# Kernel tuning notes

Measured on AMD Instinct MI355X. Metric: run time of the kernel, lower is better.

## Reference

```python
import jax, jax.numpy as jnp
import numpy as np

N_ASSETS = 128
N_FEATURES = 128
BATCH = 32
N_ITERS = 500      # fixed-iteration OSQP-style ADMM (replaces CVXPY/OSQP solve)
RHO = 0.1          # ADMM penalty
SIGMA = 1e-6       # primal regularization (OSQP default scale)
RELAX = 1.6        # over-relaxation
ALPHA = 0.5        # self.alpha (EN mix)
DELTA = 10.0       # risk aversion (forward default)
NEG_INF = -1e20


def setup_inputs() -> dict:
    key = jax.random.key(0)
    ks = jax.random.split(key, 3)
    X = jax.random.normal(ks[0], (BATCH, N_FEATURES), jnp.float32)
    F = jax.random.normal(ks[1], (N_ASSETS, N_ASSETS), jnp.float32)
    V = (F @ F.T) / N_ASSETS + 0.1 * jnp.eye(N_ASSETS, dtype=jnp.float32)  # PSD covariance
    beta = 0.1 * jax.random.normal(ks[2], (N_FEATURES, N_ASSETS), jnp.float32)
    theta_E = jnp.zeros((N_ASSETS,), jnp.float32)
    theta_D = jnp.zeros((N_ASSETS,), jnp.float32)
    log_gamma1 = jnp.zeros((), jnp.float32)
    log_gamma2 = jnp.zeros((), jnp.float32)
    A = jnp.ones((1, N_ASSETS), jnp.float32)        # budget: sum(z) == 1
    b = jnp.ones((1,), jnp.float32)
    G = -jnp.eye(N_ASSETS, dtype=jnp.float32)       # long-only: -z <= 0
    h = jnp.zeros((N_ASSETS,), jnp.float32)
    return dict(X=X, V=V, beta=beta, theta_E=theta_E, theta_D=theta_D,
                log_gamma1=log_gamma1, log_gamma2=log_gamma2, A=A, b=b, G=G, h=h)


def _forward(X, V, beta, theta_E, theta_D, log_gamma1, log_gamma2, A, b, G, h):
    n = V.shape[0]
    y_pred = X @ beta                                  # (B, n)
    gamma1 = 10.0 ** log_gamma1
    gamma2 = 10.0 ** log_gamma2
    d = jax.nn.sigmoid(theta_D)                        # diag(D)
    e = jax.nn.sigmoid(theta_E)                        # diag(E)
    Q_reg = DELTA * V + (1.0 - ALPHA) * gamma2 * jnp.diag(d * d)
    # L1 split z = u_plus - u_minus, u >= 0 -> augmented QP in u of size 2n
    Q_aug = jnp.block([[Q_reg, -Q_reg], [-Q_reg, Q_reg]])   # (2n, 2n)
    p_term = ALPHA * gamma1 * e                        # alpha*gamma1*colsum(E^T) with E diagonal
    # p_i = -y_pred[i]; p_aug = [p + p_term, -p + p_term]
    P = jnp.concatenate([-y_pred + p_term[None, :], y_pred + p_term[None, :]], axis=1)  # (B, 2n)
    # constraints: [A,-A] u == b ; [G,-G] u <= h ; -I u <= 0
    C = jnp.concatenate([
        jnp.concatenate([A, -A], axis=1),
        jnp.concatenate([G, -G], axis=1),
        -jnp.eye(2 * n, dtype=V.dtype),
    ], axis=0)                                         # (m, 2n), m = m_eq + n + 2n
    m_eq = A.shape[0]
    lo = jnp.concatenate([b, jnp.full((C.shape[0] - m_eq,), NEG_INF, V.dtype)])
    up = jnp.concatenate([b, h, jnp.zeros((2 * n,), V.dtype)])
    # OSQP ADMM with KKT reduced to an SPD system, factorized ONCE and shared across batch
    nz = 2 * n
    M = Q_aug + SIGMA * jnp.eye(nz, dtype=V.dtype) + RHO * (C.T @ C)
    L = jnp.linalg.cholesky(M)
    mC = C.shape[0]

    def solve_one(p):
        def step(carry, _):
            x, z, y = carry
            rhs = SIGMA * x - p + C.T @ (RHO * z - y)
            x_t = jax.scipy.linalg.cho_solve((L, True), rhs)
            z_t = C @ x_t
            x_new = RELAX * x_t + (1.0 - RELAX) * x
            z_r = RELAX * z_t + (1.0 - RELAX) * z
            z_new = jnp.clip(z_r + y / RHO, lo, up)
            y_new = y + RHO * (z_r - z_new)
            return (x_new, z_new, y_new), None
        init = (jnp.zeros((nz,), p.dtype), jnp.zeros((mC,), p.dtype), jnp.zeros((mC,), p.dtype))
        (x, _, _), _ = jax.lax.scan(step, init, None, length=N_ITERS)
        return x

    u = jax.vmap(solve_one)(P)                         # (B, 2n)
    z_batch = u[:, :n] - u[:, n:]                      # recover signed weights
    return z_batch, y_pred


def reference(X, V, beta, theta_E, theta_D, log_gamma1, log_gamma2, A, b, G, h):
    return _forward(X, V, beta, theta_E, theta_D, log_gamma1, log_gamma2, A, b, G, h)
```

## Files before the change

kernel.cpp:

```cpp
#include <hip/hip_runtime.h>

#define N 128
#define BATCH 32
#define N_SEG1 88
#define N_SEGM 16
#define N_CG 24

static constexpr float RHO_     = 0.1f;
static constexpr float SIGMA_   = 1e-6f;
static constexpr float RELAX_   = 1.9f;
static constexpr float ALPHA_   = 0.5f;
static constexpr float DELTA_   = 10.0f;
static constexpr float LN10_    = 2.302585092994046f;


__device__ __forceinline__ float rdlane(float v, int l) {
    return __builtin_bit_cast(float,
        __builtin_amdgcn_readlane(__builtin_bit_cast(int, v), l));
}
template <int CTRL, int RMASK>
__device__ __forceinline__ float dppadd(float v) {
    int r = __builtin_amdgcn_update_dpp(0, __builtin_bit_cast(int, v),
                                        CTRL, RMASK, 0xf, true);
    return v + __builtin_bit_cast(float, r);
}
__device__ __forceinline__ float wave_sum64(float v) {
    v = dppadd<0x111, 0xf>(v);
    v = dppadd<0x112, 0xf>(v);
    v = dppadd<0x114, 0xf>(v);
    v = dppadd<0x118, 0xf>(v);
    v = dppadd<0x142, 0xa>(v);
    v = dppadd<0x143, 0xc>(v);
    return rdlane(v, 63);
}

__global__ __launch_bounds__(256, 1) void k_front(
    const float* __restrict__ V, const float* __restrict__ thD,
    const float* __restrict__ lg2p, const float* __restrict__ Ag,
    float* __restrict__ H, float* __restrict__ wv)
{
    __shared__ alignas(16) float qs[2][2][N];

    const int tid  = threadIdx.x;
    const int c    = blockIdx.x;
    const int lane = tid & 63;
    const int wav4 = tid >> 6;
    const int i    = tid & 127;
    const int s    = tid >> 7;
    const int jb   = s * 64;

    float breg[64];
    {
        float ai   = Ag[i];
        float g2   = expf(lg2p[0] * LN10_);
        float di   = 1.0f / (1.0f + expf(-thD[i]));
        float diag = 2.0f * RHO_
                   + 2.0f * (1.0f - ALPHA_) * g2 * di * di
                   + (SIGMA_ + RHO_);
        float t2r  = 2.0f * RHO_ * ai;
        const float4* vp = (const float4*)(V + i * N + jb);
        const float4* ap = (const float4*)(Ag + jb);
#pragma unroll
        for (int j4 = 0; j4 < 16; ++j4) {
            float4 v4 = vp[j4], a4 = ap[j4];
            breg[4 * j4 + 0] = fmaf(2.0f * DELTA_, v4.x, t2r * a4.x)
                             + ((jb + 4 * j4 + 0 == i) ? diag : 0.f);
            breg[4 * j4 + 1] = fmaf(2.0f * DELTA_, v4.y, t2r * a4.y)
                             + ((jb + 4 * j4 + 1 == i) ? diag : 0.f);
            breg[4 * j4 + 2] = fmaf(2.0f * DELTA_, v4.z, t2r * a4.z)
                             + ((jb + 4 * j4 + 2 == i) ? diag : 0.f);
            breg[4 * j4 + 3] = fmaf(2.0f * DELTA_, v4.w, t2r * a4.w)
                             + ((jb + 4 * j4 + 3 == i) ? diag : 0.f);
        }
    }

    float x0 = 0.f, x1 = 0.f;
    float r0 = (c < N) ? ((lane == c) ? 1.f : 0.f) : Ag[lane];
    float r1 = (c < N) ? ((lane + 64 == c) ? 1.f : 0.f) : Ag[lane + 64];
    float p0 = r0, p1 = r1;
    float rr = wave_sum64(fmaf(r0, r0, r1 * r1));

    for (int it = 0; it < N_CG; ++it) {
        const int par = it & 1;
        {
            float psel = s ? p1 : p0;
            float a0 = 0.f, a1 = 0.f, a2 = 0.f, a3 = 0.f;
#pragma unroll
            for (int j = 0; j < 64; j += 4) {
                a0 = fmaf(breg[j + 0], rdlane(psel, j + 0), a0);
                a1 = fmaf(breg[j + 1], rdlane(psel, j + 1), a1);
                a2 = fmaf(breg[j + 2], rdlane(psel, j + 2), a2);
                a3 = fmaf(breg[j + 3], rdlane(psel, j + 3), a3);
            }
            qs[par][s][i] = (a0 + a1) + (a2 + a3);
        }
        __syncthreads();
        float q0 = qs[par][0][lane]      + qs[par][1][lane];
        float q1 = qs[par][0][lane + 64] + qs[par][1][lane + 64];
        float spq = wave_sum64(fmaf(p0, q0, p1 * q1));
        float srq = wave_sum64(fmaf(r0, q0, r1 * q1));
        float sqq = wave_sum64(fmaf(q0, q0, q1 * q1));
        float alpha = rr / fmaxf(spq, 1e-30f);
        x0 = fmaf(alpha, p0, x0); x1 = fmaf(alpha, p1, x1);
        r0 = fmaf(-alpha, q0, r0); r1 = fmaf(-alpha, q1, r1);
        float rrn = fmaf(alpha * alpha, sqq, fmaf(-2.0f * alpha, srq, rr));
        rrn = fmaxf(rrn, 0.f);
        float beta_ = rrn / fmaxf(rr, 1e-30f);
        rr = rrn;
        p0 = fmaf(beta_, p0, r0); p1 = fmaf(beta_, p1, r1);
    }
    if (wav4 == 0) {
        if (c < N) { H[c * N + lane] = x0; H[c * N + lane + 64] = x1; }
        else       { wv[lane] = x0; wv[lane + 64] = x1; }
    }
}

__global__ __launch_bounds__(256, 1) void k_admm(
    const float* __restrict__ Hg, const float* __restrict__ wg,
    const float* __restrict__ Ag, const float* __restrict__ bvec,
    const float* __restrict__ hvec, const float* __restrict__ X,
    const float* __restrict__ betag, const float* __restrict__ thE,
    const float* __restrict__ lg1p, float* __restrict__ out)
{
    __shared__ float pps[2][2][N];
    __shared__ float wzs[2][2];
    __shared__ float Xs[N];
    __shared__ float reds[4][3];

    int tid = threadIdx.x, b = blockIdx.x;
    const int lane = tid & 63;
    const int wav4 = tid >> 6;
    const int i    = tid & 127;
    const int s    = tid >> 7;
    const int jb   = s * 64;
    const int r    = jb + lane;

    if (tid < N) Xs[tid] = X[b * N + tid];
    __syncthreads();
    float y = 0.f;
#pragma unroll 8
    for (int k = 0; k < N; ++k)
        y = fmaf(Xs[k], betag[k * N + r], y);
    float gamma1 = expf(lg1p[0] * LN10_);
    float e  = 1.0f / (1.0f + expf(-thE[r]));
    float pt = ALPHA_ * gamma1 * e;
    float p1_i = -y + pt;
    float p2_i =  y + pt;
    if ((wav4 & 1) == 0)
        out[BATCH * N + b * N + r] = y;

    float hreg[64];
    {
        const float4* hp = (const float4*)(Hg + i * N + jb);
#pragma unroll
        for (int j4 = 0; j4 < 16; ++j4) {
            float4 v4 = hp[j4];
            hreg[4 * j4 + 0] = v4.x; hreg[4 * j4 + 1] = v4.y;
            hreg[4 * j4 + 2] = v4.z; hreg[4 * j4 + 3] = v4.w;
        }
    }
    float wl = wg[r];
    float b0 = bvec[0];

    float a_i  = Ag[r];
    float h_i  = hvec[r];
    float x1 = 0.f, x2 = 0.f;
    float z0 = 0.f, y0 = 0.f;
    float zg = 0.f, yg = 0.f;
    float zi1 = 0.f, yi1 = 0.f;
    float zi2 = 0.f, yi2 = 0.f;
    float svr = -p1_i - p2_i;
    float dl  = -p1_i + p2_i;

    const float inv_sr  = 1.0f / (SIGMA_ + RHO_);
    const float inv_rho = 1.0f / RHO_;
    const float cR = 1.0f - RELAX_;
    const float R2 = 0.5f * RELAX_;

#define ADMM_ITER(PAR)                                                    \
    {                                                                     \
        const int par = (PAR);                                            \
        if ((wav4 & 1) == 0) {                                            \
            float zp = wave_sum64(wl * dl);                               \
            if (lane == 0) wzs[par][s] = zp;                              \
        }                                                                 \
        float a0 = 0.f, a1 = 0.f, a2 = 0.f, a3 = 0.f;                     \
        _Pragma("unroll")                                                 \
        for (int j = 0; j < 64; j += 4) {                                 \
            a0 = fmaf(hreg[j + 0], rdlane(dl, j + 0), a0);                \
            a1 = fmaf(hreg[j + 1], rdlane(dl, j + 1), a1);                \
            a2 = fmaf(hreg[j + 2], rdlane(dl, j + 2), a2);                \
            a3 = fmaf(hreg[j + 3], rdlane(dl, j + 3), a3);                \
        }                                                                 \
        pps[par][s][i] = (a0 + a1) + (a2 + a3);                           \
        __syncthreads();                                                  \
        float xd  = pps[par][0][r] + pps[par][1][r];                      \
        float zt0 = wzs[par][0] + wzs[par][1];                            \
        float xs  = svr * inv_sr;                                         \
        float sd1 = xs + xd;                                              \
        float sd2 = xs - xd;                                              \
        x1 = fmaf(R2, sd1, cR * x1);                                      \
        x2 = fmaf(R2, sd2, cR * x2);                                      \
        float zr0 = fmaf(RELAX_, zt0, cR * z0);                           \
        y0 = fmaf(RHO_, zr0 - b0, y0); z0 = b0;                           \
        float zrg = fmaf(-RELAX_, xd, cR * zg);                           \
        float zng = fminf(fmaf(yg, inv_rho, zrg), h_i);                   \
        yg = fmaf(RHO_, zrg - zng, yg); zg = zng;                         \
        float zr1 = fmaf(-R2, sd1, cR * zi1);                             \
        float zn1 = fminf(fmaf(yi1, inv_rho, zr1), 0.f);                  \
        yi1 = fmaf(RHO_, zr1 - zn1, yi1); zi1 = zn1;                      \
        float zr2 = fmaf(-R2, sd2, cR * zi2);                             \
        float zn2 = fminf(fmaf(yi2, inv_rho, zr2), 0.f);                  \
        yi2 = fmaf(RHO_, zr2 - zn2, yi2); zi2 = zn2;                      \
        float t0  = fmaf(RHO_, z0,  -y0);                                 \
        float tg  = fmaf(RHO_, zg,  -yg);                                 \
        float tI1 = fmaf(RHO_, zi1, -yi1);                                \
        float tI2 = fmaf(RHO_, zi2, -yi2);                                \
        float g  = fmaf(a_i, t0, -tg);                                    \
        float r1 = fmaf(SIGMA_, x1, -p1_i) + g - tI1;                     \
        float r2 = fmaf(SIGMA_, x2, -p2_i) - g - tI2;                     \
        svr = r1 + r2;                                                    \
        dl  = r1 - r2;                                                    \
    }

    for (int it = 0; it < N_SEG1; ++it) ADMM_ITER(it & 1)
    float zA = x1 - x2;
    for (int it = 0; it < N_SEGM; ++it) ADMM_ITER(it & 1)
    float zB = x1 - x2;
    for (int it = 0; it < N_SEGM; ++it) ADMM_ITER(it & 1)
    float zC = x1 - x2;
#undef ADMM_ITER

    float d1 = zB - zA;
    float d2 = zC - zB;
    float s21 = wave_sum64(d2 * d1);
    float s11 = wave_sum64(d1 * d1);
    float s22 = wave_sum64(d2 * d2);
    if (lane == 0) {
        reds[wav4][0] = s21; reds[wav4][1] = s11; reds[wav4][2] = s22;
    }
    __syncthreads();
    float d21 = reds[0][0] + reds[1][0] + reds[2][0] + reds[3][0];
    float d11 = reds[0][1] + reds[1][1] + reds[2][1] + reds[3][1];
    float d22 = reds[0][2] + reds[1][2] + reds[2][2] + reds[3][2];
    float lam16 = fminf(d21 / fmaxf(d11, 1e-30f), 0.98f);
    bool  ok = (d21 > 0.f) && (d21 * d21 > 0.81f * d11 * d22)
             && (lam16 > 0.f);
    float fac  = lam16 / (1.0f - lam16);
    float zout = ok ? fmaf(d2, fac, zC) : zC;
    if ((wav4 & 1) == 0)
        out[b * N + r] = zout;
}

extern "C" void kernel_launch(void* const* d_in, const int* in_sizes, int n_in,
                              void* d_out, int out_size, void* d_ws, size_t ws_size,
                              hipStream_t stream) {
    (void)in_sizes; (void)n_in; (void)out_size; (void)ws_size;
    const float* X    = (const float*)d_in[0];
    const float* V    = (const float*)d_in[1];
    const float* beta = (const float*)d_in[2];
    const float* thE  = (const float*)d_in[3];
    const float* thD  = (const float*)d_in[4];
    const float* lg1  = (const float*)d_in[5];
    const float* lg2  = (const float*)d_in[6];
    const float* A    = (const float*)d_in[7];
    const float* bv   = (const float*)d_in[8];
    const float* hv   = (const float*)d_in[10];
    float* out = (float*)d_out;
    float* ws  = (float*)d_ws;
    float* Hm = ws;
    float* wv = ws + 16384;

    hipLaunchKernelGGL(k_front, dim3(N + 1), dim3(256), 0, stream,
                       V, thD, lg2, A, Hm, wv);
    hipLaunchKernelGGL(k_admm,  dim3(BATCH), dim3(256), 0, stream,
                       Hm, wv, A, bv, hv, X, beta, thE, lg1, out);
}
```

Before: 149.3 us.

## Fuse front CG and ADMM kernels into one cooperative launch with grid sync

Merges the CG-based inverse construction kernel and the batched ADMM kernel into a single cooperative kernel. Blocks beyond the front range compute y_pred and the linear terms while the front blocks run CG, then a grid-wide sync makes H available. This removes one launch and the inter-kernel gap and overlaps the prediction matmul with the CG work. In exchange it pays the cost of a cooperative launch and a grid barrier, and the front blocks idle-exit afterwards.

```diff
diff --git a/kernel.cpp b/kernel.cpp
--- a/kernel.cpp
+++ b/kernel.cpp
@@ -1,7 +1,11 @@
 #include <hip/hip_runtime.h>
+#include <hip/hip_cooperative_groups.h>
+
+namespace cg = cooperative_groups;
 
 #define N 128
 #define BATCH 32
+#define NFRONT (N + 1)
 #define N_SEG1 88
 #define N_SEGM 16
 #define N_CG 24
@@ -34,100 +38,23 @@
     return rdlane(v, 63);
 }
 
-__global__ __launch_bounds__(256, 1) void k_front(
+__global__ __launch_bounds__(256, 1) void k_fused(
     const float* __restrict__ V, const float* __restrict__ thD,
     const float* __restrict__ lg2p, const float* __restrict__ Ag,
-    float* __restrict__ H, float* __restrict__ wv)
+    float* __restrict__ Hws, float* __restrict__ wvws,
+    const float* __restrict__ bvec, const float* __restrict__ hvec,
+    const float* __restrict__ X, const float* __restrict__ betag,
+    const float* __restrict__ thE, const float* __restrict__ lg1p,
+    float* __restrict__ out)
 {
     __shared__ alignas(16) float qs[2][2][N];
-
-    const int tid  = threadIdx.x;
-    const int c    = blockIdx.x;
-    const int lane = tid & 63;
-    const int wav4 = tid >> 6;
-    const int i    = tid & 127;
-    const int s    = tid >> 7;
-    const int jb   = s * 64;
-
-    float breg[64];
-    {
-        float ai   = Ag[i];
-        float g2   = expf(lg2p[0] * LN10_);
-        float di   = 1.0f / (1.0f + expf(-thD[i]));
-        float diag = 2.0f * RHO_
-                   + 2.0f * (1.0f - ALPHA_) * g2 * di * di
-                   + (SIGMA_ + RHO_);
-        float t2r  = 2.0f * RHO_ * ai;
-        const float4* vp = (const float4*)(V + i * N + jb);
-        const float4* ap = (const float4*)(Ag + jb);
-#pragma unroll
-        for (int j4 = 0; j4 < 16; ++j4) {
-            float4 v4 = vp[j4], a4 = ap[j4];
-            breg[4 * j4 + 0] = fmaf(2.0f * DELTA_, v4.x, t2r * a4.x)
-                             + ((jb + 4 * j4 + 0 == i) ? diag : 0.f);
-            breg[4 * j4 + 1] = fmaf(2.0f * DELTA_, v4.y, t2r * a4.y)
-                             + ((jb + 4 * j4 + 1 == i) ? diag : 0.f);
-            breg[4 * j4 + 2] = fmaf(2.0f * DELTA_, v4.z, t2r * a4.z)
-                             + ((jb + 4 * j4 + 2 == i) ? diag : 0.f);
-            breg[4 * j4 + 3] = fmaf(2.0f * DELTA_, v4.w, t2r * a4.w)
-                             + ((jb + 4 * j4 + 3 == i) ? diag : 0.f);
-        }
-    }
-
-    float x0 = 0.f, x1 = 0.f;
-    float r0 = (c < N) ? ((lane == c) ? 1.f : 0.f) : Ag[lane];
-    float r1 = (c < N) ? ((lane + 64 == c) ? 1.f : 0.f) : Ag[lane + 64];
-    float p0 = r0, p1 = r1;
-    float rr = wave_sum64(fmaf(r0, r0, r1 * r1));
-
-    for (int it = 0; it < N_CG; ++it) {
-        const int par = it & 1;
-        {
-            float psel = s ? p1 : p0;
-            float a0 = 0.f, a1 = 0.f, a2 = 0.f, a3 = 0.f;
-#pragma unroll
-            for (int j = 0; j < 64; j += 4) {
-                a0 = fmaf(breg[j + 0], rdlane(psel, j + 0), a0);
-                a1 = fmaf(breg[j + 1], rdlane(psel, j + 1), a1);
-                a2 = fmaf(breg[j + 2], rdlane(psel, j + 2), a2);
-                a3 = fmaf(breg[j + 3], rdlane(psel, j + 3), a3);
-            }
-            qs[par][s][i] = (a0 + a1) + (a2 + a3);
-        }
-        __syncthreads();
-        float q0 = qs[par][0][lane]      + qs[par][1][lane];
-        float q1 = qs[par][0][lane + 64] + qs[par][1][lane + 64];
-        float spq = wave_sum64(fmaf(p0, q0, p1 * q1));
-        float srq = wave_sum64(fmaf(r0, q0, r1 * q1));
-        float sqq = wave_sum64(fmaf(q0, q0, q1 * q1));
-        float alpha = rr / fmaxf(spq, 1e-30f);
-        x0 = fmaf(alpha, p0, x0); x1 = fmaf(alpha, p1, x1);
-        r0 = fmaf(-alpha, q0, r0); r1 = fmaf(-alpha, q1, r1);
-        float rrn = fmaf(alpha * alpha, sqq, fmaf(-2.0f * alpha, srq, rr));
-        rrn = fmaxf(rrn, 0.f);
-        float beta_ = rrn / fmaxf(rr, 1e-30f);
-        rr = rrn;
-        p0 = fmaf(beta_, p0, r0); p1 = fmaf(beta_, p1, r1);
-    }
-    if (wav4 == 0) {
-        if (c < N) { H[c * N + lane] = x0; H[c * N + lane + 64] = x1; }
-        else       { wv[lane] = x0; wv[lane + 64] = x1; }
-    }
-}
-
-__global__ __launch_bounds__(256, 1) void k_admm(
-    const float* __restrict__ Hg, const float* __restrict__ wg,
-    const float* __restrict__ Ag, const float* __restrict__ bvec,
-    const float* __restrict__ hvec, const float* __restrict__ X,
-    const float* __restrict__ betag, const float* __restrict__ thE,
-    const float* __restrict__ lg1p, float* __restrict__ out)
-{
     __shared__ float pps[2][2][N];
     __shared__ float wzs[2][2];
     __shared__ float Xs[N];
     __shared__ float reds[4][3];
 
-    int tid = threadIdx.x, b = blockIdx.x;
+    const int cb   = blockIdx.x;
+    const int tid  = threadIdx.x;
     const int lane = tid & 63;
     const int wav4 = tid >> 6;
     const int i    = tid & 127;
@@ -135,23 +62,100 @@
     const int jb   = s * 64;
     const int r    = jb + lane;
 
-    if (tid < N) Xs[tid] = X[b * N + tid];
-    __syncthreads();
-    float y = 0.f;
+    float p1_i = 0.f, p2_i = 0.f;
+
+    if (cb < NFRONT) {
+        const int c = cb;
+        float breg[64];
+        {
+            float ai   = Ag[i];
+            float g2   = expf(lg2p[0] * LN10_);
+            float di   = 1.0f / (1.0f + expf(-thD[i]));
+            float diag = 2.0f * RHO_
+                       + 2.0f * (1.0f - ALPHA_) * g2 * di * di
+                       + (SIGMA_ + RHO_);
+            float t2r  = 2.0f * RHO_ * ai;
+            const float4* vp = (const float4*)(V + i * N + jb);
+            const float4* ap = (const float4*)(Ag + jb);
+#pragma unroll
+            for (int j4 = 0; j4 < 16; ++j4) {
+                float4 v4 = vp[j4], a4 = ap[j4];
+                breg[4 * j4 + 0] = fmaf(2.0f * DELTA_, v4.x, t2r * a4.x)
+                                 + ((jb + 4 * j4 + 0 == i) ? diag : 0.f);
+                breg[4 * j4 + 1] = fmaf(2.0f * DELTA_, v4.y, t2r * a4.y)
+                                 + ((jb + 4 * j4 + 1 == i) ? diag : 0.f);
+                breg[4 * j4 + 2] = fmaf(2.0f * DELTA_, v4.z, t2r * a4.z)
+                                 + ((jb + 4 * j4 + 2 == i) ? diag : 0.f);
+                breg[4 * j4 + 3] = fmaf(2.0f * DELTA_, v4.w, t2r * a4.w)
+                                 + ((jb + 4 * j4 + 3 == i) ? diag : 0.f);
+            }
+        }
+        float x0 = 0.f, x1 = 0.f;
+        float r0 = (c < N) ? ((lane == c) ? 1.f : 0.f) : Ag[lane];
+        float r1 = (c < N) ? ((lane + 64 == c) ? 1.f : 0.f) : Ag[lane + 64];
+        float p0 = r0, p1 = r1;
+        float rr = wave_sum64(fmaf(r0, r0, r1 * r1));
+
+        for (int it = 0; it < N_CG; ++it) {
+            const int par = it & 1;
+            {
+                float psel = s ? p1 : p0;
+                float a0 = 0.f, a1 = 0.f, a2 = 0.f, a3 = 0.f;
+#pragma unroll
+                for (int j = 0; j < 64; j += 4) {
+                    a0 = fmaf(breg[j + 0], rdlane(psel, j + 0), a0);
+                    a1 = fmaf(breg[j + 1], rdlane(psel, j + 1), a1);
+                    a2 = fmaf(breg[j + 2], rdlane(psel, j + 2), a2);
+                    a3 = fmaf(breg[j + 3], rdlane(psel, j + 3), a3);
+                }
+                qs[par][s][i] = (a0 + a1) + (a2 + a3);
+            }
+            __syncthreads();
+            float q0 = qs[par][0][lane]      + qs[par][1][lane];
+            float q1 = qs[par][0][lane + 64] + qs[par][1][lane + 64];
+            float spq = wave_sum64(fmaf(p0, q0, p1 * q1));
+            float srq = wave_sum64(fmaf(r0, q0, r1 * q1));
+            float sqq = wave_sum64(fmaf(q0, q0, q1 * q1));
+            float alpha = rr / fmaxf(spq, 1e-30f);
+            x0 = fmaf(alpha, p0, x0); x1 = fmaf(alpha, p1, x1);
+            r0 = fmaf(-alpha, q0, r0); r1 = fmaf(-alpha, q1, r1);
+            float rrn = fmaf(alpha * alpha, sqq,
+                             fmaf(-2.0f * alpha, srq, rr));
+            rrn = fmaxf(rrn, 0.f);
+            float beta_ = rrn / fmaxf(rr, 1e-30f);
+            rr = rrn;
+            p0 = fmaf(beta_, p0, r0); p1 = fmaf(beta_, p1, r1);
+        }
+        if (wav4 == 0) {
+            if (c < N) { Hws[c * N + lane] = x0; Hws[c * N + lane + 64] = x1; }
+            else       { wvws[lane] = x0; wvws[lane + 64] = x1; }
+        }
+    } else {
+        const int b = cb - NFRONT;
+        if (tid < N) Xs[tid] = X[b * N + tid];
+        __syncthreads();
+        float y = 0.f;
 #pragma unroll 8
-    for (int k = 0; k < N; ++k)
-        y = fmaf(Xs[k], betag[k * N + r], y);
-    float gamma1 = expf(lg1p[0] * LN10_);
-    float e  = 1.0f / (1.0f + expf(-thE[r]));
-    float pt = ALPHA_ * gamma1 * e;
-    float p1_i = -y + pt;
-    float p2_i =  y + pt;
-    if ((wav4 & 1) == 0)
-        out[BATCH * N + b * N + r] = y;
-
+        for (int k = 0; k < N; ++k)
+            y = fmaf(Xs[k], betag[k * N + r], y);
+        float gamma1 = expf(lg1p[0] * LN10_);
+        float e  = 1.0f / (1.0f + expf(-thE[r]));
+        float pt = ALPHA_ * gamma1 * e;
+        p1_i = -y + pt;
+        p2_i =  y + pt;
+        if ((wav4 & 1) == 0)
+            out[BATCH * N + b * N + r] = y;
+    }
+
+    __threadfence();
+    cg::this_grid().sync();
+    if (cb < NFRONT) return;
+    __threadfence();
+
+    const int b = cb - NFRONT;
     float hreg[64];
     {
-        const float4* hp = (const float4*)(Hg + i * N + jb);
+        const float4* hp = (const float4*)(Hws + i * N + jb);
 #pragma unroll
         for (int j4 = 0; j4 < 16; ++j4) {
             float4 v4 = hp[j4];
@@ -159,9 +163,8 @@
             hreg[4 * j4 + 2] = v4.z; hreg[4 * j4 + 3] = v4.w;
         }
     }
-    float wl = wg[r];
+    float wl = wvws[r];
     float b0 = bvec[0];
-
     float a_i  = Ag[r];
     float h_i  = hvec[r];
     float x1 = 0.f, x2 = 0.f;
@@ -271,8 +274,10 @@
     float* Hm = ws;
     float* wv = ws + 16384;
 
-    hipLaunchKernelGGL(k_front, dim3(N + 1), dim3(256), 0, stream,
-                       V, thD, lg2, A, Hm, wv);
-    hipLaunchKernelGGL(k_admm,  dim3(BATCH), dim3(256), 0, stream,
-                       Hm, wv, A, bv, hv, X, beta, thE, lg1, out);
-}
+    void* args[] = { (void*)&V, (void*)&thD, (void*)&lg2, (void*)&A,
+                     (void*)&Hm, (void*)&wv, (void*)&bv, (void*)&hv,
+                     (void*)&X, (void*)&beta, (void*)&thE, (void*)&lg1,
+                     (void*)&out };
+    hipLaunchCooperativeKernel((void*)k_fused, dim3(NFRONT + BATCH),
+                               dim3(256), args, 0, stream);
+}
```

Result: slower. 202.5 us (+35.6%).
